# Kernel optimization log

Hardware: AMD Instinct MI355X
Metric: run time of the kernel (lower is better)

The kernel has to match this reference:

```python
import jax, jax.numpy as jnp
import numpy as np

B, S, D, H, T, R = 2, 2048, 768, 12, 64, 50
DH = D // H
EPS = 1e-12


def setup_inputs() -> dict:
    key = jax.random.key(0)
    ks = jax.random.split(key, 12)
    w = lambda k, shape: jax.random.normal(k, shape, jnp.float32) * 0.02
    inp = {
        "hidden_states": jax.random.normal(ks[0], (B, S, D), jnp.float32),
        "tag_emb": w(ks[1], (T, D)),
        "sa_wq": w(ks[2], (D, D)), "sa_bq": jnp.zeros((D,), jnp.float32),
        "sa_wk": w(ks[3], (D, D)), "sa_bk": jnp.zeros((D,), jnp.float32),
        "sa_wv": w(ks[4], (D, D)), "sa_bv": jnp.zeros((D,), jnp.float32),
        "sa_wo": w(ks[5], (D, D)), "sa_bo": jnp.zeros((D,), jnp.float32),
        "sa_ln_g": jnp.ones((D,), jnp.float32), "sa_ln_b": jnp.zeros((D,), jnp.float32),
        "ca_wq": w(ks[6], (D, D)), "ca_bq": jnp.zeros((D,), jnp.float32),
        "ca_wk": w(ks[7], (D, D)), "ca_bk": jnp.zeros((D,), jnp.float32),
        "ca_wv": w(ks[8], (D, D)), "ca_bv": jnp.zeros((D,), jnp.float32),
        "ca_wo": w(ks[9], (D, D)), "ca_bo": jnp.zeros((D,), jnp.float32),
        "ca_ln_g": jnp.ones((D,), jnp.float32), "ca_ln_b": jnp.zeros((D,), jnp.float32),
        "ff_w1": w(ks[10], (D, 3072)), "ff_b1": jnp.zeros((3072,), jnp.float32),
        "ff_w2": w(ks[11], (3072, D)), "ff_b2": jnp.zeros((D,), jnp.float32),
        "ff_ln_g": jnp.ones((D,), jnp.float32), "ff_ln_b": jnp.zeros((D,), jnp.float32),
    }
    return inp


def _layernorm(x, g, b):
    m = jnp.mean(x, axis=-1, keepdims=True)
    v = jnp.mean(jnp.square(x - m), axis=-1, keepdims=True)
    return (x - m) * jax.lax.rsqrt(v + EPS) * g + b


def _bert_attention(x, kv, mask, wq, bq, wk, bk, wv, bv, wo, bo, ln_g, ln_b):
    # BertSelfAttention: multi-head attn; mask (if any) is ADDED to scores (HF semantics).
    Bq, Sq = x.shape[0], x.shape[1]
    Sk = kv.shape[1]
    q = (x @ wq + bq).reshape(Bq, Sq, H, DH)
    k = (kv @ wk + bk).reshape(Bq, Sk, H, DH)
    v = (kv @ wv + bv).reshape(Bq, Sk, H, DH)
    scores = jnp.einsum("bqhd,bkhd->bhqk", q, k) / jnp.sqrt(jnp.float32(DH))
    if mask is not None:
        scores = scores + mask  # additive 0/1 band mask, as in the source
    probs = jax.nn.softmax(scores, axis=-1)
    ctx = jnp.einsum("bhqk,bkhd->bqhd", probs, v).reshape(Bq, Sq, D)
    # BertSelfOutput: dense + residual + LayerNorm
    return _layernorm(ctx @ wo + bo + x, ln_g, ln_b)


def reference(hidden_states, tag_emb,
              sa_wq, sa_bq, sa_wk, sa_bk, sa_wv, sa_bv, sa_wo, sa_bo, sa_ln_g, sa_ln_b,
              ca_wq, ca_bq, ca_wk, ca_bk, ca_wv, ca_bv, ca_wo, ca_bo, ca_ln_g, ca_ln_b,
              ff_w1, ff_b1, ff_w2, ff_b2, ff_ln_g, ff_ln_b):
    Sd = hidden_states.shape[1]
    # banded mask: tril(+R) * triu(-R) -> 1 inside window, 0 outside (added to scores)
    i = jnp.arange(Sd)
    band = (jnp.abs(i[:, None] - i[None, :]) <= R).astype(hidden_states.dtype)  # [S,S]
    attn_out = _bert_attention(hidden_states, hidden_states, band,
                               sa_wq, sa_bq, sa_wk, sa_bk, sa_wv, sa_bv,
                               sa_wo, sa_bo, sa_ln_g, sa_ln_b)
    tags = jnp.broadcast_to(tag_emb[None], (hidden_states.shape[0], T, D))
    attn_out = _bert_attention(attn_out, tags, None,
                               ca_wq, ca_bq, ca_wk, ca_bk, ca_wv, ca_bv,
                               ca_wo, ca_bo, ca_ln_g, ca_ln_b)
    # BertIntermediate + BertOutput (exact erf gelu as in HF)
    inter = jax.nn.gelu(attn_out @ ff_w1 + ff_b1, approximate=False)
    return _layernorm(inter @ ff_w2 + ff_b2 + attn_out, ff_ln_g, ff_ln_b)
```

## Files before the change

kernel.cpp:

```cpp
#include <hip/hip_runtime.h>
#include <cstdint>
#include <cstddef>


typedef __bf16 bf16;
typedef __bf16 bf16x8 __attribute__((ext_vector_type(8)));
typedef __bf16 bf16x4 __attribute__((ext_vector_type(4)));
typedef __bf16 bf16x2 __attribute__((ext_vector_type(2)));
typedef float  floatx4 __attribute__((ext_vector_type(4)));

__device__ __forceinline__ void glds16(const bf16* g, bf16* l) {
  __builtin_amdgcn_global_load_lds((const __attribute__((address_space(1))) void*)g,
                                   (__attribute__((address_space(3))) void*)l, 16, 0, 0);
}

__device__ __forceinline__ float fexp2(float x) {
  float r;
  asm("v_exp_f32 %0, %1" : "=v"(r) : "v"(x));
  return r;
}

__global__ __launch_bounds__(256) void k_concat3(const float* __restrict__ a,
                                                 const float* __restrict__ b,
                                                 const float* __restrict__ c,
                                                 float* __restrict__ o, int seg) {
  int i = blockIdx.x * 256 + threadIdx.x;
  int s = i / seg, j = i - s * seg;
  const float* p = s == 0 ? a : (s == 1 ? b : c);
  o[i] = p[j];
}

__global__ void k_pad_tags(const float* __restrict__ tag, bf16* __restrict__ out) {
  int i = blockIdx.x * 256 + threadIdx.x;
  if (i < 64 * 768) out[i] = (bf16)tag[i];
  else if (i < 128 * 768) out[i] = (bf16)0.f;
}

__global__ __launch_bounds__(256) void k_transpose(const float* __restrict__ W,
                                                   bf16* __restrict__ Wt,
                                                   int K, int N) {
  __shared__ bf16 tile[64][72];
  int n0 = blockIdx.x * 64, k0 = blockIdx.y * 64;
  int t = threadIdx.x;
  int r = t >> 2, cg = (t & 3) * 16;
  const float* src = W + (size_t)(k0 + r) * N + n0 + cg;
  float tmp[16];
  *(float4*)&tmp[0]  = *(const float4*)(src);
  *(float4*)&tmp[4]  = *(const float4*)(src + 4);
  *(float4*)&tmp[8]  = *(const float4*)(src + 8);
  *(float4*)&tmp[12] = *(const float4*)(src + 12);
#pragma unroll
  for (int i = 0; i < 16; ++i) tile[r][cg + i] = (bf16)tmp[i];
  __syncthreads();
  bf16* dst = Wt + (size_t)(n0 + r) * K + k0 + cg;
#pragma unroll
  for (int g = 0; g < 2; ++g) {
    bf16x8 pack;
#pragma unroll
    for (int i = 0; i < 8; ++i) pack[i] = tile[cg + g * 8 + i][r];
    *(bf16x8*)(dst + g * 8) = pack;
  }
}

__global__ __launch_bounds__(256) void k_transpose4(const float* __restrict__ W0,
                                                    const float* __restrict__ W1,
                                                    const float* __restrict__ W2w,
                                                    const float* __restrict__ W3,
                                                    bf16* __restrict__ Wt) {
  __shared__ bf16 tile[64][72];
  int z = blockIdx.z;
  const float* W = z == 0 ? W0 : (z == 1 ? W1 : (z == 2 ? W2w : W3));
  bf16* dstb = Wt + (size_t)z * 768 * 768;
  int n0 = blockIdx.x * 64, k0 = blockIdx.y * 64;
  int t = threadIdx.x;
  int r = t >> 2, cg = (t & 3) * 16;
  const float* src = W + (size_t)(k0 + r) * 768 + n0 + cg;
  float tmp[16];
  *(float4*)&tmp[0]  = *(const float4*)(src);
  *(float4*)&tmp[4]  = *(const float4*)(src + 4);
  *(float4*)&tmp[8]  = *(const float4*)(src + 8);
  *(float4*)&tmp[12] = *(const float4*)(src + 12);
#pragma unroll
  for (int i = 0; i < 16; ++i) tile[r][cg + i] = (bf16)tmp[i];
  __syncthreads();
  bf16* dst = dstb + (size_t)(n0 + r) * 768 + k0 + cg;
#pragma unroll
  for (int g = 0; g < 2; ++g) {
    bf16x8 pack;
#pragma unroll
    for (int i = 0; i < 8; ++i) pack[i] = tile[cg + g * 8 + i][r];
    *(bf16x8*)(dst + g * 8) = pack;
  }
}

template <int BM, int KS, bool AF32, bool CF32>
__global__ __launch_bounds__(256) void k_gemm(const void* __restrict__ Av,
                                              const bf16* __restrict__ Bt,
                                              const float* __restrict__ bias,
                                              void* __restrict__ Cv,
                                              int M, int N, int K, int act) {
  constexpr int MT = BM / 32;
  __shared__ bf16 As[KS][BM * 32];
  __shared__ bf16 Bs[KS][128 * 32];
  int tid = threadIdx.x;
  int lane = tid & 63, wave = tid >> 6;
  int l16 = lane & 15, quad = lane >> 4;
  int wm = wave & 1, wn = wave >> 1;
  int m0 = blockIdx.x * BM, n0 = blockIdx.y * 128;
  int arow = tid >> 2, acol = (tid & 3) * 8;
  int ldst = arow * 32 + acol;

  const bf16* Ab = (const bf16*)Av;
  const float* Af = (const float*)Av;
  const bf16* Ap = Ab + (size_t)(m0 + arow) * K + acol;
  const float* Apf = Af + (size_t)(m0 + arow) * K + acol;
  const bf16* Bp = Bt + (size_t)(n0 + arow) * K + acol;

  floatx4 acc[MT][4];
#pragma unroll
  for (int i = 0; i < MT; ++i)
#pragma unroll
    for (int j = 0; j < 4; ++j) acc[i][j] = floatx4{0.f, 0.f, 0.f, 0.f};

  float4 p0a, p0b, p1a, p1b;
  if constexpr (AF32) {
    p0a = *(const float4*)(Apf);
    p0b = *(const float4*)(Apf + 4);
    p1a = *(const float4*)(Apf + (size_t)64 * K);
    p1b = *(const float4*)(Apf + (size_t)64 * K + 4);
  }

  for (int k = 0; k < K; k += 32 * KS) {
    __syncthreads();
#pragma unroll
    for (int ks = 0; ks < KS; ++ks) {
      glds16(Bp + k + ks * 32, &Bs[ks][ldst]);
      glds16(Bp + (size_t)64 * K + k + ks * 32, &Bs[ks][ldst + 2048]);
    }
    if constexpr (AF32) {
      bf16x8 c0, c1;
      c0[0] = (bf16)p0a.x; c0[1] = (bf16)p0a.y; c0[2] = (bf16)p0a.z; c0[3] = (bf16)p0a.w;
      c0[4] = (bf16)p0b.x; c0[5] = (bf16)p0b.y; c0[6] = (bf16)p0b.z; c0[7] = (bf16)p0b.w;
      c1[0] = (bf16)p1a.x; c1[1] = (bf16)p1a.y; c1[2] = (bf16)p1a.z; c1[3] = (bf16)p1a.w;
      c1[4] = (bf16)p1b.x; c1[5] = (bf16)p1b.y; c1[6] = (bf16)p1b.z; c1[7] = (bf16)p1b.w;
      *(bf16x8*)&As[0][ldst] = c0;
      *(bf16x8*)&As[0][ldst + 2048] = c1;
    } else {
#pragma unroll
      for (int ks = 0; ks < KS; ++ks) {
        glds16(Ap + k + ks * 32, &As[ks][ldst]);
        if constexpr (BM == 128) glds16(Ap + (size_t)64 * K + k + ks * 32, &As[ks][ldst + 2048]);
      }
    }
    __syncthreads();
    if constexpr (AF32) {
      if (k + 32 < K) {
        p0a = *(const float4*)(Apf + k + 32);
        p0b = *(const float4*)(Apf + k + 36);
        p1a = *(const float4*)(Apf + (size_t)64 * K + k + 32);
        p1b = *(const float4*)(Apf + (size_t)64 * K + k + 36);
      }
    }
#pragma unroll
    for (int ks = 0; ks < KS; ++ks) {
      bf16x8 a_frag[MT], b_frag[4];
#pragma unroll
      for (int mt = 0; mt < MT; ++mt)
        a_frag[mt] = *(const bf16x8*)&As[ks][(wm * (BM / 2) + mt * 16 + l16) * 32 + quad * 8];
#pragma unroll
      for (int nt = 0; nt < 4; ++nt)
        b_frag[nt] = *(const bf16x8*)&Bs[ks][(wn * 64 + nt * 16 + l16) * 32 + quad * 8];
#pragma unroll
      for (int mt = 0; mt < MT; ++mt)
#pragma unroll
        for (int nt = 0; nt < 4; ++nt)
          acc[mt][nt] = __builtin_amdgcn_mfma_f32_16x16x32_bf16(a_frag[mt], b_frag[nt], acc[mt][nt], 0, 0, 0);
    }
  }

#pragma unroll
  for (int nt = 0; nt < 4; ++nt) {
    int col = n0 + wn * 64 + nt * 16 + l16;
    float bv = bias[col];
#pragma unroll
    for (int mt = 0; mt < MT; ++mt) {
#pragma unroll
      for (int r = 0; r < 4; ++r) {
        int row = m0 + wm * (BM / 2) + mt * 16 + quad * 4 + r;
        float v = acc[mt][nt][r] + bv;
        if (act) v = 0.5f * v * (1.f + erff(v * 0.70710678118654752f));
        if constexpr (CF32) ((float*)Cv)[(size_t)row * N + col] = v;
        else ((bf16*)Cv)[(size_t)row * N + col] = (bf16)v;
      }
    }
  }
}

__global__ __launch_bounds__(256) void k_attn_mfma(const bf16* __restrict__ Q, int ldq,
                                                   const bf16* __restrict__ Kp,
                                                   const bf16* __restrict__ Vp, int ldkv,
                                                   bf16* __restrict__ O,
                                                   int S, int Skv,
                                                   long long kv_bstride, int bandR) {
  const int NH = 12;
  int qt = blockIdx.x, bh = blockIdx.y;
  int bb = bh / NH, h = bh % NH;
  const bf16* Qb = Q + (size_t)bb * S * ldq + h * 64;
  const bf16* Kb = Kp + (size_t)bb * kv_bstride + h * 64;
  const bf16* Vb = Vp + (size_t)bb * kv_bstride + h * 64;
  bf16* Ob = O + (size_t)bb * S * 768 + h * 64;

  __shared__ __align__(16) char smem[47104];
  float* Obuf = (float*)smem;
  float* l0_arr = (float*)(smem + 16896);

  int tid = threadIdx.x, wave = tid >> 6, lane = tid & 63;
  int quad = lane >> 4, l16 = lane & 15;
  int qh = wave & 1, kh = wave >> 1;
  bf16 (*Psw)[40] = (bf16(*)[40])(smem + 36864 + wave * 2560);

  const float C1 = 0.18033688f;
  const float C2 = 1.44269504f;

  int r = tid >> 2, cg = (tid & 3) * 16;
  int vk0 = 2 * (tid & 31);
  int vd0 = 8 * (tid >> 5);
  int vcol = (vk0 + 16 * (vd0 >> 4)) & 63;

  bf16x8 aq[2][2];
#pragma unroll
  for (int mt = 0; mt < 2; ++mt) {
    const bf16* qsrc = Qb + (size_t)(qt * 64 + qh * 32 + mt * 16 + l16) * ldq;
#pragma unroll
    for (int ks = 0; ks < 2; ++ks) {
      bf16x8 t = *(const bf16x8*)(qsrc + ks * 32 + quad * 8);
#pragma unroll
      for (int e = 0; e < 8; ++e) t[e] = (bf16)((float)t[e] * C1);
      aq[mt][ks] = t;
    }
  }

  bf16x8 kr0, kr1, vr0, vr1;
  {
    const bf16* ksrc = Kb + (size_t)r * ldkv + cg;
    kr0 = *(const bf16x8*)ksrc;
    kr1 = *(const bf16x8*)(ksrc + 8);
    const bf16* vsrc = Vb + (size_t)vk0 * ldkv + vd0;
    vr0 = *(const bf16x8*)vsrc;
    vr1 = *(const bf16x8*)(vsrc + ldkv);
  }

  float l_part[2][4];
  floatx4 acc[2][4];
#pragma unroll
  for (int mt = 0; mt < 2; ++mt)
#pragma unroll
    for (int j = 0; j < 4; ++j) {
      l_part[mt][j] = 0.f;
      acc[mt][j] = floatx4{0.f, 0.f, 0.f, 0.f};
    }

  int qi0 = qt * 64 + qh * 32 + quad * 4;

  for (int kc = 0; kc < Skv; kc += 64) {
    int cur = (kc >> 6) & 1;
    bf16 (*Ks)[72] = (bf16(*)[72])(smem + cur * 9216);
    bf16 (*Vt)[72] = (bf16(*)[72])(smem + 18432 + cur * 9216);
    *(bf16x8*)&Ks[r][cg] = kr0;
    *(bf16x8*)&Ks[r][cg + 8] = kr1;
#pragma unroll
    for (int e = 0; e < 8; ++e) {
      bf16x2 p; p[0] = vr0[e]; p[1] = vr1[e];
      *(bf16x2*)&Vt[vd0 + e][vcol] = p;
    }
    if (kc + 64 < Skv) {
      const bf16* ksrc = Kb + (size_t)(kc + 64 + r) * ldkv + cg;
      kr0 = *(const bf16x8*)ksrc;
      kr1 = *(const bf16x8*)(ksrc + 8);
      const bf16* vsrc = Vb + (size_t)(kc + 64 + vk0) * ldkv + vd0;
      vr0 = *(const bf16x8*)vsrc;
      vr1 = *(const bf16x8*)(vsrc + ldkv);
    }
    __syncthreads();

    floatx4 s[2][2];
    __builtin_amdgcn_s_setprio(1);
#pragma unroll
    for (int kt = 0; kt < 2; ++kt) {
      bf16x8 bk0 = *(const bf16x8*)&Ks[kh * 32 + kt * 16 + l16][quad * 8];
      bf16x8 bk1 = *(const bf16x8*)&Ks[kh * 32 + kt * 16 + l16][32 + quad * 8];
#pragma unroll
      for (int mt = 0; mt < 2; ++mt) {
        floatx4 c = {0.f, 0.f, 0.f, 0.f};
        c = __builtin_amdgcn_mfma_f32_16x16x32_bf16(aq[mt][0], bk0, c, 0, 0, 0);
        c = __builtin_amdgcn_mfma_f32_16x16x32_bf16(aq[mt][1], bk1, c, 0, 0, 0);
        s[mt][kt] = c;
      }
    }
    __builtin_amdgcn_s_setprio(0);

    bool masked = (bandR >= 0) && (kc <= qt * 64 + 63 + bandR) &&
                  (kc + 63 >= qt * 64 - bandR);
    if (masked) {
#pragma unroll
      for (int kt = 0; kt < 2; ++kt) {
        int kj = kc + kh * 32 + kt * 16 + l16;
        int colp = (kt * 16 + l16 + 8 * quad) & 31;
#pragma unroll
        for (int mt = 0; mt < 2; ++mt)
#pragma unroll
          for (int rr = 0; rr < 4; ++rr) {
            int d = qi0 + mt * 16 + rr - kj; if (d < 0) d = -d;
            float e = fexp2(s[mt][kt][rr] + (d <= bandR ? C2 : 0.f));
            l_part[mt][rr] += e;
            Psw[mt * 16 + quad * 4 + rr][colp] = (bf16)e;
          }
      }
    } else {
#pragma unroll
      for (int kt = 0; kt < 2; ++kt) {
        int colp = (kt * 16 + l16 + 8 * quad) & 31;
#pragma unroll
        for (int mt = 0; mt < 2; ++mt)
#pragma unroll
          for (int rr = 0; rr < 4; ++rr) {
            float e = fexp2(s[mt][kt][rr]);
            l_part[mt][rr] += e;
            Psw[mt * 16 + quad * 4 + rr][colp] = (bf16)e;
          }
      }
    }

    bf16x8 ap[2];
#pragma unroll
    for (int mt = 0; mt < 2; ++mt)
      ap[mt] = *(const bf16x8*)&Psw[mt * 16 + l16][8 * ((quad + (l16 >> 2)) & 3)];
    __builtin_amdgcn_s_setprio(1);
#pragma unroll
    for (int nt = 0; nt < 4; ++nt) {
      bf16x8 bv = *(const bf16x8*)&Vt[nt * 16 + l16][(kh * 32 + quad * 8 + 16 * nt) & 63];
#pragma unroll
      for (int mt = 0; mt < 2; ++mt)
        acc[mt][nt] = __builtin_amdgcn_mfma_f32_16x16x32_bf16(ap[mt], bv, acc[mt][nt], 0, 0, 0);
    }
    __builtin_amdgcn_s_setprio(0);
  }

  float lr[2][4];
#pragma unroll
  for (int mt = 0; mt < 2; ++mt)
#pragma unroll
    for (int rr = 0; rr < 4; ++rr) {
      float t = l_part[mt][rr];
      t += __shfl_xor(t, 1);
      t += __shfl_xor(t, 2);
      t += __shfl_xor(t, 4);
      t += __shfl_xor(t, 8);
      lr[mt][rr] = t;
    }
  __syncthreads();
  if (kh == 0) {
#pragma unroll
    for (int mt = 0; mt < 2; ++mt)
#pragma unroll
      for (int nt = 0; nt < 4; ++nt)
#pragma unroll
        for (int rr = 0; rr < 4; ++rr)
          Obuf[(qh * 32 + mt * 16 + quad * 4 + rr) * 66 + nt * 16 + l16] = acc[mt][nt][rr];
    if (l16 == 0) {
#pragma unroll
      for (int mt = 0; mt < 2; ++mt)
#pragma unroll
        for (int rr = 0; rr < 4; ++rr)
          l0_arr[qh * 32 + mt * 16 + quad * 4 + rr] = lr[mt][rr];
    }
  }
  __syncthreads();
  if (kh == 1) {
#pragma unroll
    for (int mt = 0; mt < 2; ++mt)
#pragma unroll
      for (int rr = 0; rr < 4; ++rr) {
        int ql = qh * 32 + mt * 16 + quad * 4 + rr;
        float lt = lr[mt][rr] + l0_arr[ql];
        int qrow = qt * 64 + ql;
#pragma unroll
        for (int nt = 0; nt < 4; ++nt) {
          float o = (acc[mt][nt][rr] + Obuf[ql * 66 + nt * 16 + l16]) / lt;
          Ob[(size_t)qrow * 768 + nt * 16 + l16] = (bf16)o;
        }
      }
  }
}

template <typename TY, typename TR, typename TO>
__global__ __launch_bounds__(256) void k_add_ln(const TY* __restrict__ Y,
                                                const TR* __restrict__ X,
                                                const float* __restrict__ g,
                                                const float* __restrict__ b,
                                                TO* __restrict__ out) {
  int wave = threadIdx.x >> 6, lane = threadIdx.x & 63;
  int row = blockIdx.x * 4 + wave;
  const TY* y = Y + (size_t)row * 768;
  const TR* x = X + (size_t)row * 768;
  float v[12];
  float s = 0.f, s2 = 0.f;
#pragma unroll
  for (int c = 0; c < 3; ++c) {
    int idx = c * 256 + lane * 4;
    float yv[4], xv[4];
    if constexpr (__is_same(TY, float)) {
      float4 t = *(const float4*)(y + idx);
      yv[0] = t.x; yv[1] = t.y; yv[2] = t.z; yv[3] = t.w;
    } else {
      bf16x4 t = *(const bf16x4*)(y + idx);
#pragma unroll
      for (int i = 0; i < 4; ++i) yv[i] = (float)t[i];
    }
    if constexpr (__is_same(TR, float)) {
      float4 t = *(const float4*)(x + idx);
      xv[0] = t.x; xv[1] = t.y; xv[2] = t.z; xv[3] = t.w;
    } else {
      bf16x4 t = *(const bf16x4*)(x + idx);
#pragma unroll
      for (int i = 0; i < 4; ++i) xv[i] = (float)t[i];
    }
#pragma unroll
    for (int i = 0; i < 4; ++i) {
      float t = yv[i] + xv[i];
      v[c * 4 + i] = t; s += t; s2 += t * t;
    }
  }
#pragma unroll
  for (int off = 32; off > 0; off >>= 1) { s += __shfl_xor(s, off); s2 += __shfl_xor(s2, off); }
  float mean = s * (1.f / 768.f);
  float var = fmaxf(s2 * (1.f / 768.f) - mean * mean, 0.f);
  float inv = rsqrtf(var + 1e-12f);
  TO* o = out + (size_t)row * 768;
#pragma unroll
  for (int c = 0; c < 3; ++c) {
    int idx = c * 256 + lane * 4;
    float4 gv = *(const float4*)(g + idx);
    float4 bv = *(const float4*)(b + idx);
    float r0 = (v[c * 4 + 0] - mean) * inv * gv.x + bv.x;
    float r1 = (v[c * 4 + 1] - mean) * inv * gv.y + bv.y;
    float r2 = (v[c * 4 + 2] - mean) * inv * gv.z + bv.z;
    float r3 = (v[c * 4 + 3] - mean) * inv * gv.w + bv.w;
    if constexpr (__is_same(TO, float)) {
      float4 ov = {r0, r1, r2, r3};
      *(float4*)(o + idx) = ov;
    } else {
      bf16x4 ov;
      ov[0] = (bf16)r0; ov[1] = (bf16)r1; ov[2] = (bf16)r2; ov[3] = (bf16)r3;
      *(bf16x4*)(o + idx) = ov;
    }
  }
}

extern "C" void kernel_launch(void* const* d_in, const int* in_sizes, int n_in,
                              void* d_out, int out_size, void* d_ws, size_t ws_size,
                              hipStream_t stream) {
  (void)in_sizes; (void)n_in; (void)out_size; (void)ws_size;
  const float* X     = (const float*)d_in[0];
  const float* tag   = (const float*)d_in[1];
  const float* sa_wq = (const float*)d_in[2];
  const float* sa_bq = (const float*)d_in[3];
  const float* sa_wk = (const float*)d_in[4];
  const float* sa_bk = (const float*)d_in[5];
  const float* sa_wv = (const float*)d_in[6];
  const float* sa_bv = (const float*)d_in[7];
  const float* sa_wo = (const float*)d_in[8];
  const float* sa_bo = (const float*)d_in[9];
  const float* sa_lg = (const float*)d_in[10];
  const float* sa_lb = (const float*)d_in[11];
  const float* ca_wq = (const float*)d_in[12];
  const float* ca_bq = (const float*)d_in[13];
  const float* ca_wk = (const float*)d_in[14];
  const float* ca_bk = (const float*)d_in[15];
  const float* ca_wv = (const float*)d_in[16];
  const float* ca_bv = (const float*)d_in[17];
  const float* ca_wo = (const float*)d_in[18];
  const float* ca_bo = (const float*)d_in[19];
  const float* ca_lg = (const float*)d_in[20];
  const float* ca_lb = (const float*)d_in[21];
  const float* ff_w1 = (const float*)d_in[22];
  const float* ff_b1 = (const float*)d_in[23];
  const float* ff_w2 = (const float*)d_in[24];
  const float* ff_b2 = (const float*)d_in[25];
  const float* ff_lg = (const float*)d_in[26];
  const float* ff_lb = (const float*)d_in[27];

  float* outf = (float*)d_out;
  bf16* outb = (bf16*)d_out;
  const size_t SLOT = (size_t)4096 * 768;

  bf16* BIG   = (bf16*)d_ws;
  bf16* slotA = BIG + (size_t)4096 * 2304;
  bf16* Wall  = slotA + SLOT;
  bf16* W2    = Wall + (size_t)3072 * 768;
  bf16* tagp  = W2;
  bf16* k2v2  = W2 + (size_t)128 * 768;
  float* bQKV = (float*)(W2 + (size_t)128 * 768 + (size_t)128 * 1536);
  float* bKV2 = bQKV + 2304;

  dim3 blk(256);

  k_concat3<<<dim3(9), blk, 0, stream>>>(sa_bq, sa_bk, sa_bv, bQKV, 768);
  k_concat3<<<dim3(6), blk, 0, stream>>>(ca_bk, ca_bv, nullptr, bKV2, 768);
  k_pad_tags<<<dim3(384), blk, 0, stream>>>(tag, tagp);

  k_transpose4<<<dim3(12, 12, 4), blk, 0, stream>>>(sa_wq, sa_wk, sa_wv, sa_wo, Wall);
  k_gemm<128, 1, true, false><<<dim3(32, 18), blk, 0, stream>>>(X, Wall, bQKV, BIG,
                                                                4096, 2304, 768, 0);
  k_attn_mfma<<<dim3(32, 24), blk, 0, stream>>>(BIG, 2304, BIG + 768, BIG + 1536, 2304,
                                                outb, 2048, 2048, (long long)2048 * 2304, 50);
  k_gemm<64, 2, false, false><<<dim3(64, 6), blk, 0, stream>>>(outb, Wall + (size_t)2304 * 768,
                                                               sa_bo, slotA, 4096, 768, 768, 0);
  k_add_ln<bf16, float, bf16><<<dim3(1024), blk, 0, stream>>>(slotA, X, sa_lg, sa_lb, slotA);

  k_transpose4<<<dim3(12, 12, 4), blk, 0, stream>>>(ca_wq, ca_wk, ca_wv, ca_wo, Wall);
  k_gemm<64, 2, false, false><<<dim3(64, 6), blk, 0, stream>>>(slotA, Wall, ca_bq, BIG,
                                                               4096, 768, 768, 0);
  k_gemm<64, 2, false, false><<<dim3(2, 12), blk, 0, stream>>>(tagp, Wall + (size_t)768 * 768,
                                                               bKV2, k2v2, 128, 1536, 768, 0);
  k_attn_mfma<<<dim3(32, 24), blk, 0, stream>>>(BIG, 768, k2v2, k2v2 + 768, 1536,
                                                outb, 2048, 64, 0, -1);
  k_gemm<64, 2, false, false><<<dim3(64, 6), blk, 0, stream>>>(outb, Wall + (size_t)2304 * 768,
                                                               ca_bo, BIG + SLOT, 4096, 768, 768, 0);
  k_add_ln<bf16, bf16, bf16><<<dim3(1024), blk, 0, stream>>>(BIG + SLOT, slotA, ca_lg, ca_lb, slotA);

  k_transpose<<<dim3(48, 12), blk, 0, stream>>>(ff_w1, Wall, 768, 3072);
  k_transpose<<<dim3(12, 48), blk, 0, stream>>>(ff_w2, W2, 3072, 768);
  for (int mc = 0; mc < 2; ++mc) {
    const bf16* a2 = slotA + (size_t)mc * 2048 * 768;
    float* yo = outf + (size_t)mc * 2048 * 768;
    k_gemm<128, 2, false, false><<<dim3(16, 24), blk, 0, stream>>>(a2, Wall, ff_b1, BIG,
                                                                   2048, 3072, 768, 1);
    k_gemm<64, 2, false, true><<<dim3(32, 6), blk, 0, stream>>>(BIG, W2, ff_b2, yo,
                                                                2048, 768, 3072, 0);
    k_add_ln<float, bf16, float><<<dim3(512), blk, 0, stream>>>(yo, a2, ff_lg, ff_lb, yo);
  }
}
```

Before: 465.7 us.

## Shrink GEMM tiles and split-K the FFN down-projection to raise occupancy

New measurement: 397.1 us. -14.7%, faster.

```diff
diff --git a/kernel.cpp b/kernel.cpp
--- a/kernel.cpp
+++ b/kernel.cpp
@@ -93,41 +93,46 @@
   }
 }
 
-template <int BM, int KS, bool AF32, bool CF32>
+template <int BM, int BN, int KS, bool AF32, bool CF32>
 __global__ __launch_bounds__(256) void k_gemm(const void* __restrict__ Av,
                                               const bf16* __restrict__ Bt,
                                               const float* __restrict__ bias,
                                               void* __restrict__ Cv,
-                                              int M, int N, int K, int act) {
+                                              void* __restrict__ Cv2,
+                                              int M, int N, int K, int ld, int act) {
   constexpr int MT = BM / 32;
+  constexpr int NT = BN / 32;
   __shared__ bf16 As[KS][BM * 32];
-  __shared__ bf16 Bs[KS][128 * 32];
+  __shared__ bf16 Bs[KS][BN * 32];
   int tid = threadIdx.x;
   int lane = tid & 63, wave = tid >> 6;
   int l16 = lane & 15, quad = lane >> 4;
   int wm = wave & 1, wn = wave >> 1;
-  int m0 = blockIdx.x * BM, n0 = blockIdx.y * 128;
+  int m0 = blockIdx.x * BM, n0 = blockIdx.y * BN;
+  int z = blockIdx.z;
   int arow = tid >> 2, acol = (tid & 3) * 8;
   int ldst = arow * 32 + acol;
 
   const bf16* Ab = (const bf16*)Av;
   const float* Af = (const float*)Av;
-  const bf16* Ap = Ab + (size_t)(m0 + arow) * K + acol;
-  const float* Apf = Af + (size_t)(m0 + arow) * K + acol;
-  const bf16* Bp = Bt + (size_t)(n0 + arow) * K + acol;
-
-  floatx4 acc[MT][4];
+  const bf16* Ap = Ab + (size_t)(m0 + arow) * ld + z * K + acol;
+  const float* Apf = Af + (size_t)(m0 + arow) * ld + acol;
+  const bf16* Bp = Bt + (size_t)(n0 + arow) * ld + z * K + acol;
+
+  floatx4 acc[MT][NT];
 #pragma unroll
   for (int i = 0; i < MT; ++i)
 #pragma unroll
-    for (int j = 0; j < 4; ++j) acc[i][j] = floatx4{0.f, 0.f, 0.f, 0.f};
+    for (int j = 0; j < NT; ++j) acc[i][j] = floatx4{0.f, 0.f, 0.f, 0.f};
 
   float4 p0a, p0b, p1a, p1b;
   if constexpr (AF32) {
     p0a = *(const float4*)(Apf);
     p0b = *(const float4*)(Apf + 4);
-    p1a = *(const float4*)(Apf + (size_t)64 * K);
-    p1b = *(const float4*)(Apf + (size_t)64 * K + 4);
+    if constexpr (BM == 128) {
+      p1a = *(const float4*)(Apf + (size_t)64 * ld);
+      p1b = *(const float4*)(Apf + (size_t)64 * ld + 4);
+    }
   }
 
   for (int k = 0; k < K; k += 32 * KS) {
@@ -135,21 +140,24 @@
 #pragma unroll
     for (int ks = 0; ks < KS; ++ks) {
       glds16(Bp + k + ks * 32, &Bs[ks][ldst]);
-      glds16(Bp + (size_t)64 * K + k + ks * 32, &Bs[ks][ldst + 2048]);
+      if constexpr (BN == 128) glds16(Bp + (size_t)64 * ld + k + ks * 32, &Bs[ks][ldst + 2048]);
     }
     if constexpr (AF32) {
-      bf16x8 c0, c1;
+      bf16x8 c0;
       c0[0] = (bf16)p0a.x; c0[1] = (bf16)p0a.y; c0[2] = (bf16)p0a.z; c0[3] = (bf16)p0a.w;
       c0[4] = (bf16)p0b.x; c0[5] = (bf16)p0b.y; c0[6] = (bf16)p0b.z; c0[7] = (bf16)p0b.w;
-      c1[0] = (bf16)p1a.x; c1[1] = (bf16)p1a.y; c1[2] = (bf16)p1a.z; c1[3] = (bf16)p1a.w;
-      c1[4] = (bf16)p1b.x; c1[5] = (bf16)p1b.y; c1[6] = (bf16)p1b.z; c1[7] = (bf16)p1b.w;
       *(bf16x8*)&As[0][ldst] = c0;
-      *(bf16x8*)&As[0][ldst + 2048] = c1;
+      if constexpr (BM == 128) {
+        bf16x8 c1;
+        c1[0] = (bf16)p1a.x; c1[1] = (bf16)p1a.y; c1[2] = (bf16)p1a.z; c1[3] = (bf16)p1a.w;
+        c1[4] = (bf16)p1b.x; c1[5] = (bf16)p1b.y; c1[6] = (bf16)p1b.z; c1[7] = (bf16)p1b.w;
+        *(bf16x8*)&As[0][ldst + 2048] = c1;
+      }
     } else {
 #pragma unroll
       for (int ks = 0; ks < KS; ++ks) {
         glds16(Ap + k + ks * 32, &As[ks][ldst]);
-        if constexpr (BM == 128) glds16(Ap + (size_t)64 * K + k + ks * 32, &As[ks][ldst + 2048]);
+        if constexpr (BM == 128) glds16(Ap + (size_t)64 * ld + k + ks * 32, &As[ks][ldst + 2048]);
       }
     }
     __syncthreads();
@@ -157,31 +165,34 @@
       if (k + 32 < K) {
         p0a = *(const float4*)(Apf + k + 32);
         p0b = *(const float4*)(Apf + k + 36);
-        p1a = *(const float4*)(Apf + (size_t)64 * K + k + 32);
-        p1b = *(const float4*)(Apf + (size_t)64 * K + k + 36);
+        if constexpr (BM == 128) {
+          p1a = *(const float4*)(Apf + (size_t)64 * ld + k + 32);
+          p1b = *(const float4*)(Apf + (size_t)64 * ld + k + 36);
+        }
       }
     }
 #pragma unroll
     for (int ks = 0; ks < KS; ++ks) {
-      bf16x8 a_frag[MT], b_frag[4];
+      bf16x8 a_frag[MT], b_frag[NT];
 #pragma unroll
       for (int mt = 0; mt < MT; ++mt)
         a_frag[mt] = *(const bf16x8*)&As[ks][(wm * (BM / 2) + mt * 16 + l16) * 32 + quad * 8];
 #pragma unroll
-      for (int nt = 0; nt < 4; ++nt)
-        b_frag[nt] = *(const bf16x8*)&Bs[ks][(wn * 64 + nt * 16 + l16) * 32 + quad * 8];
+      for (int nt = 0; nt < NT; ++nt)
+        b_frag[nt] = *(const bf16x8*)&Bs[ks][(wn * (BN / 2) + nt * 16 + l16) * 32 + quad * 8];
 #pragma unroll
       for (int mt = 0; mt < MT; ++mt)
 #pragma unroll
-        for (int nt = 0; nt < 4; ++nt)
+        for (int nt = 0; nt < NT; ++nt)
           acc[mt][nt] = __builtin_amdgcn_mfma_f32_16x16x32_bf16(a_frag[mt], b_frag[nt], acc[mt][nt], 0, 0, 0);
     }
   }
 
-#pragma unroll
-  for (int nt = 0; nt < 4; ++nt) {
-    int col = n0 + wn * 64 + nt * 16 + l16;
-    float bv = bias[col];
+  void* Co = (z == 0) ? Cv : Cv2;
+#pragma unroll
+  for (int nt = 0; nt < NT; ++nt) {
+    int col = n0 + wn * (BN / 2) + nt * 16 + l16;
+    float bv = (z == 0) ? bias[col] : 0.f;
 #pragma unroll
     for (int mt = 0; mt < MT; ++mt) {
 #pragma unroll
@@ -189,8 +200,8 @@
         int row = m0 + wm * (BM / 2) + mt * 16 + quad * 4 + r;
         float v = acc[mt][nt][r] + bv;
         if (act) v = 0.5f * v * (1.f + erff(v * 0.70710678118654752f));
-        if constexpr (CF32) ((float*)Cv)[(size_t)row * N + col] = v;
-        else ((bf16*)Cv)[(size_t)row * N + col] = (bf16)v;
+        if constexpr (CF32) ((float*)Co)[(size_t)row * N + col] = v;
+        else ((bf16*)Co)[(size_t)row * N + col] = (bf16)v;
       }
     }
   }
@@ -396,6 +407,7 @@
 template <typename TY, typename TR, typename TO>
 __global__ __launch_bounds__(256) void k_add_ln(const TY* __restrict__ Y,
                                                 const TR* __restrict__ X,
+                                                const float* __restrict__ Y2,
                                                 const float* __restrict__ g,
                                                 const float* __restrict__ b,
                                                 TO* __restrict__ out) {
@@ -424,6 +436,10 @@
       bf16x4 t = *(const bf16x4*)(x + idx);
 #pragma unroll
       for (int i = 0; i < 4; ++i) xv[i] = (float)t[i];
+    }
+    if (Y2 != nullptr) {
+      float4 t2 = *(const float4*)(Y2 + (size_t)row * 768 + idx);
+      xv[0] += t2.x; xv[1] += t2.y; xv[2] += t2.z; xv[3] += t2.w;
     }
 #pragma unroll
     for (int i = 0; i < 4; ++i) {
@@ -502,6 +518,7 @@
   bf16* k2v2  = W2 + (size_t)128 * 768;
   float* bQKV = (float*)(W2 + (size_t)128 * 768 + (size_t)128 * 1536);
   float* bKV2 = bQKV + 2304;
+  float* P1   = (float*)(BIG + 2 * SLOT);
 
   dim3 blk(256);
 
@@ -510,34 +527,38 @@
   k_pad_tags<<<dim3(384), blk, 0, stream>>>(tag, tagp);
 
   k_transpose4<<<dim3(12, 12, 4), blk, 0, stream>>>(sa_wq, sa_wk, sa_wv, sa_wo, Wall);
-  k_gemm<128, 1, true, false><<<dim3(32, 18), blk, 0, stream>>>(X, Wall, bQKV, BIG,
-                                                                4096, 2304, 768, 0);
+  k_gemm<64, 128, 1, true, false><<<dim3(64, 18), blk, 0, stream>>>(X, Wall, bQKV, BIG, nullptr,
+                                                                    4096, 2304, 768, 768, 0);
   k_attn_mfma<<<dim3(32, 24), blk, 0, stream>>>(BIG, 2304, BIG + 768, BIG + 1536, 2304,
                                                 outb, 2048, 2048, (long long)2048 * 2304, 50);
-  k_gemm<64, 2, false, false><<<dim3(64, 6), blk, 0, stream>>>(outb, Wall + (size_t)2304 * 768,
-                                                               sa_bo, slotA, 4096, 768, 768, 0);
-  k_add_ln<bf16, float, bf16><<<dim3(1024), blk, 0, stream>>>(slotA, X, sa_lg, sa_lb, slotA);
+  k_gemm<64, 64, 2, false, false><<<dim3(64, 12), blk, 0, stream>>>(outb, Wall + (size_t)2304 * 768,
+                                                                    sa_bo, slotA, nullptr,
+                                                                    4096, 768, 768, 768, 0);
+  k_add_ln<bf16, float, bf16><<<dim3(1024), blk, 0, stream>>>(slotA, X, nullptr, sa_lg, sa_lb, slotA);
 
   k_transpose4<<<dim3(12, 12, 4), blk, 0, stream>>>(ca_wq, ca_wk, ca_wv, ca_wo, Wall);
-  k_gemm<64, 2, false, false><<<dim3(64, 6), blk, 0, stream>>>(slotA, Wall, ca_bq, BIG,
-                                                               4096, 768, 768, 0);
-  k_gemm<64, 2, false, false><<<dim3(2, 12), blk, 0, stream>>>(tagp, Wall + (size_t)768 * 768,
-                                                               bKV2, k2v2, 128, 1536, 768, 0);
+  k_gemm<64, 64, 2, false, false><<<dim3(64, 12), blk, 0, stream>>>(slotA, Wall, ca_bq, BIG, nullptr,
+                                                                    4096, 768, 768, 768, 0);
+  k_gemm<64, 64, 2, false, false><<<dim3(2, 24), blk, 0, stream>>>(tagp, Wall + (size_t)768 * 768,
+                                                                   bKV2, k2v2, nullptr,
+                                                                   128, 1536, 768, 768, 0);
   k_attn_mfma<<<dim3(32, 24), blk, 0, stream>>>(BIG, 768, k2v2, k2v2 + 768, 1536,
                                                 outb, 2048, 64, 0, -1);
-  k_gemm<64, 2, false, false><<<dim3(64, 6), blk, 0, stream>>>(outb, Wall + (size_t)2304 * 768,
-                                                               ca_bo, BIG + SLOT, 4096, 768, 768, 0);
-  k_add_ln<bf16, bf16, bf16><<<dim3(1024), blk, 0, stream>>>(BIG + SLOT, slotA, ca_lg, ca_lb, slotA);
+  k_gemm<64, 64, 2, false, false><<<dim3(64, 12), blk, 0, stream>>>(outb, Wall + (size_t)2304 * 768,
+                                                                    ca_bo, BIG + SLOT, nullptr,
+                                                                    4096, 768, 768, 768, 0);
+  k_add_ln<bf16, bf16, bf16><<<dim3(1024), blk, 0, stream>>>(BIG + SLOT, slotA, nullptr,
+                                                             ca_lg, ca_lb, slotA);
 
   k_transpose<<<dim3(48, 12), blk, 0, stream>>>(ff_w1, Wall, 768, 3072);
   k_transpose<<<dim3(12, 48), blk, 0, stream>>>(ff_w2, W2, 3072, 768);
   for (int mc = 0; mc < 2; ++mc) {
     const bf16* a2 = slotA + (size_t)mc * 2048 * 768;
     float* yo = outf + (size_t)mc * 2048 * 768;
-    k_gemm<128, 2, false, false><<<dim3(16, 24), blk, 0, stream>>>(a2, Wall, ff_b1, BIG,
-                                                                   2048, 3072, 768, 1);
-    k_gemm<64, 2, false, true><<<dim3(32, 6), blk, 0, stream>>>(BIG, W2, ff_b2, yo,
-                                                                2048, 768, 3072, 0);
-    k_add_ln<float, bf16, float><<<dim3(512), blk, 0, stream>>>(yo, a2, ff_lg, ff_lb, yo);
-  }
-}
+    k_gemm<64, 128, 2, false, false><<<dim3(32, 24), blk, 0, stream>>>(a2, Wall, ff_b1, BIG, nullptr,
+                                                                       2048, 3072, 768, 768, 1);
+    k_gemm<64, 64, 2, false, true><<<dim3(32, 12, 2), blk, 0, stream>>>(BIG, W2, ff_b2, yo, P1,
+                                                                        2048, 768, 1536, 3072, 0);
+    k_add_ln<float, bf16, float><<<dim3(512), blk, 0, stream>>>(yo, a2, P1, ff_lg, ff_lb, yo);
+  }
+}
```
